# Kernel optimization log

Hardware: AMD Instinct MI355X
Metric: run time of the kernel (lower is better)

The kernel has to match this reference:

```python
import jax, jax.numpy as jnp
from jax import lax
import numpy as np

KS = 5
STRIDE = 4
SCALE = 10.0
PAD = 1        # conv_transpose2d padding (hardcoded in source)
OUT_PAD = 1    # output_padding
DN = ('NCHW', 'OIHW', 'NCHW')


def _same_pad(x, ks, stride):
    # torch same_padding: pad so out = ceil(H/stride)
    H, W = x.shape[-2], x.shape[-1]
    oh = -(-H // stride); ow = -(-W // stride)
    ph = max(0, (oh - 1) * stride + ks - H)
    pw = max(0, (ow - 1) * stride + ks - W)
    return jnp.pad(x, ((0, 0), (0, 0), (ph // 2, ph - ph // 2), (pw // 2, pw - pw // 2)))


def _patches(x, ks, stride):
    # torch extract_image_patches (same padding + unfold), returned as [N, L, C, ks, ks]
    N, C, H, W = x.shape
    oh = -(-H // stride); ow = -(-W // stride)
    xp = _same_pad(x, ks, stride)
    ys = (jnp.arange(oh) * stride)[:, None] + jnp.arange(ks)[None, :]   # [oh, ks]
    xs = (jnp.arange(ow) * stride)[:, None] + jnp.arange(ks)[None, :]   # [ow, ks]
    p = xp[:, :, ys, :][:, :, :, :, xs]   # [N, C, oh, ks, ow, ks]
    return p.transpose(0, 2, 4, 1, 3, 5).reshape(N, oh * ow, C, ks, ks)


def _conv3(x, W, b):
    # BasicBlock: 3x3 conv pad 1 + bias + LeakyReLU(0.01)
    y = lax.conv_general_dilated(x, W, (1, 1), [(1, 1), (1, 1)], dimension_numbers=DN)
    return jax.nn.leaky_relu(y + b[None, :, None, None], 0.01)


def _attend(qp, kp, vp):
    # qp: [C, Hp, Wp] padded query feature; kp: [L, C, ks, ks]; vp: [L, B, ks, ks]
    kmax = jnp.max(jnp.sqrt(jnp.sum(kp * kp, axis=(1, 2, 3))))
    kn = kp / kmax
    w = lax.conv_general_dilated(qp[None], kn, (STRIDE, STRIDE), 'VALID', dimension_numbers=DN)  # [1, L, h, w]
    wn = jax.nn.softmax(w * SCALE, axis=1)
    # conv_transpose2d(wn, vp, stride=4, padding=1, output_padding=1) as lhs-dilated conv
    ker = jnp.flip(vp.transpose(1, 0, 2, 3), (2, 3))  # [B, L, ks, ks]
    lo = KS - 1 - PAD
    hi = KS - 1 - PAD + OUT_PAD
    out = lax.conv_general_dilated(wn, ker, (1, 1), [(lo, hi), (lo, hi)],
                                   lhs_dilation=(STRIDE, STRIDE), dimension_numbers=DN)
    return out[0] / 6.0


def setup_inputs() -> dict:
    key = jax.random.key(0)
    k = jax.random.split(key, 12)
    N, CIN, MID, B = 8, 64, 64, 64
    H, HL = 256, 64
    s = 0.05
    return {
        'ms':   jax.random.normal(k[0], (N, B, HL, HL), jnp.float32),
        'pan':  jax.random.normal(k[1], (N, CIN, H, H), jnp.float32),
        'pan2': jax.random.normal(k[2], (N, CIN, HL, HL), jnp.float32),
        'Wq': jax.random.normal(k[3], (MID, CIN, 3, 3), jnp.float32) * s,
        'bq': jnp.zeros((MID,), jnp.float32),
        'Wk': jax.random.normal(k[4], (MID, CIN, 3, 3), jnp.float32) * s,
        'bk': jnp.zeros((MID,), jnp.float32),
        'Wv': jax.random.normal(k[5], (B, B, 3, 3), jnp.float32) * s,
        'bv': jnp.zeros((B,), jnp.float32),
        'Wr': jax.random.normal(k[6], (B, B, 3, 3), jnp.float32) * s,
        'br': jnp.zeros((B,), jnp.float32),
    }


def reference(ms, pan, pan2, Wq, bq, Wk, bk, Wv, bv, Wr, br):
    k_fea = _conv3(pan2, Wk, bk)               # [N, MID, 64, 64]
    k_patch = _patches(k_fea, KS, STRIDE)      # [N, L=256, MID, 5, 5]
    q_fea = _conv3(pan, Wq, bq)                # [N, MID, 256, 256]
    q_pad = _same_pad(q_fea, KS, STRIDE)       # [N, MID, 257, 257]
    v_fea = _conv3(ms, Wv, bv)                 # [N, B, 64, 64]
    v_patch = _patches(v_fea, KS, STRIDE)      # [N, L, B, 5, 5]
    res = jax.vmap(_attend)(q_pad, k_patch, v_patch)  # [N, B, 256, 256]
    return _conv3(res, Wr, br)
```

## Files before the change

### kernel.cpp

```cpp
#include <hip/hip_runtime.h>
#include <math.h>

#define NB   8
#define CI   64
#define COC  64
#define HQ   256
#define HK   64
#define KS   5
#define LL   256
#define NPAD 1664
#define QP2  (257 * 264)

typedef __attribute__((ext_vector_type(8))) short bf16x8s;
typedef __attribute__((ext_vector_type(4))) float f32x4;

static __device__ __forceinline__ unsigned short f2bf(float f) {
  union { float f; unsigned u; } v; v.f = f;
  unsigned r = v.u + 0x7FFF + ((v.u >> 16) & 1);
  return (unsigned short)(r >> 16);
}
static __device__ __forceinline__ float bf2f(unsigned short h) {
  union { unsigned u; float f; } v; v.u = ((unsigned)h) << 16; return v.f;
}

__global__ void wtrans8_kernel(const float* __restrict__ Wt, float* __restrict__ Wo) {
  const int co = threadIdx.x;
  const int tap = blockIdx.x;
  const int ci = blockIdx.y;
  Wo[(((co >> 3) * 64 + ci) * 9 + tap) * 8 + (co & 7)] = Wt[(co * 64 + ci) * 9 + tap];
}

__global__ void wtrans_mfma(const float* __restrict__ Wt, unsigned short* __restrict__ wimg) {
  const int ch = blockIdx.x;
  const int tap = ch >> 1, cih = ch & 1;
  for (int idx = threadIdx.x; idx < 64 * 40; idx += 256) {
    const int co = idx / 40, s = idx - co * 40;
    unsigned short v = 0;
    if (s < 32) v = f2bf(Wt[((size_t)co * 64 + cih * 32 + s) * 9 + tap]);
    wimg[(size_t)ch * 64 * 40 + idx] = v;
  }
}

__global__ void pad_copy(const float* __restrict__ src, float* __restrict__ dst,
                         int H, int W, int S, int total) {
  const int idx = blockIdx.x * 256 + threadIdx.x;
  if (idx >= total) return;
  const int p = idx / (H * W);
  const int rem = idx - p * H * W;
  const int y = rem / W, x = rem - y * W;
  dst[((size_t)p * (H + 2) + y + 1) * S + x + 1] = src[idx];
}

__global__ void border_zero(float* __restrict__ dst, int H, int W, int S) {
  const int p = blockIdx.x;
  float* b = dst + (size_t)p * (H + 2) * S;
  for (int c = threadIdx.x; c < S; c += 256) {
    b[c] = 0.f;
    b[(size_t)(H + 1) * S + c] = 0.f;
  }
  for (int r = 1 + threadIdx.x; r <= H; r += 256) {
    b[(size_t)r * S] = 0.f;
    b[(size_t)r * S + W + 1] = 0.f;
  }
}

__global__ void pad_rci(const float* __restrict__ src, unsigned short* __restrict__ dst) {
  const int ct = blockIdx.x, g = blockIdx.y, n = blockIdx.z;
  const int c0 = ct * 66;
  __shared__ float t[64 * 68];
  const int jl = threadIdx.x & 63, cg = threadIdx.x >> 6;
  const int row = g - 1;
  const bool rok = (row >= 0 && row < 256);
  for (int ci = cg; ci < 64; ci += 4) {
    #pragma unroll
    for (int jb = 0; jb < 2; ++jb) {
      const int j = jl + jb * 64;
      if (j < 66) {
        const int x = c0 - 1 + j;
        float v = 0.f;
        if (rok && x >= 0 && x < 256)
          v = src[(((size_t)n * 64 + ci) * 256 + row) * 256 + x];
        t[ci * 68 + j] = v;
      }
    }
  }
  __syncthreads();
  const int cil = threadIdx.x & 63, cc = threadIdx.x >> 6;
  unsigned short* db = dst + (((size_t)n * 258 + g) * 264) * 64;
  for (int c = cc; c < 66; c += 4)
    db[(size_t)(c0 + c) * 64 + cil] = f2bf(t[cil * 68 + c]);
}

__global__ void rbz(unsigned short* __restrict__ resbf) {
  const int n = blockIdx.x;
  unsigned short* b = resbf + (size_t)n * 258 * 264 * 64;
  for (int idx = threadIdx.x; idx < 264 * 64; idx += 256) {
    b[idx] = 0;
    b[(size_t)257 * 264 * 64 + idx] = 0;
  }
  for (int idx = threadIdx.x; idx < 256 * 64; idx += 256) {
    const int r = idx >> 6, ci = idx & 63;
    b[((size_t)(r + 1) * 264) * 64 + ci] = 0;
    b[((size_t)(r + 1) * 264 + 257) * 64 + ci] = 0;
  }
}

__global__ void qz(unsigned short* __restrict__ qhi, unsigned short* __restrict__ qlo) {
  const int n = blockIdx.x;
  unsigned short* bh = qhi + (size_t)n * QP2 * 64;
  unsigned short* bl = qlo + (size_t)n * QP2 * 64;
  for (int g = threadIdx.x; g < 4224; g += 256) {
    ((unsigned long long*)(bh + (size_t)256 * 264 * 64))[g] = 0ull;
    ((unsigned long long*)(bl + (size_t)256 * 264 * 64))[g] = 0ull;
  }
  for (int g = threadIdx.x; g < 4096; g += 256) {
    const int r = g >> 4, q = g & 15;
    const size_t off = ((size_t)r * 264 + 256) * 64 + q * 4;
    *(unsigned long long*)(bh + off) = 0ull;
    *(unsigned long long*)(bl + off) = 0ull;
  }
}

__global__ __launch_bounds__(256) void conv3m(
    const unsigned short* __restrict__ inbf,
    const unsigned short* __restrict__ wimg,
    const float* __restrict__ bias,
    float* __restrict__ out, int PS, int RS) {
  const int x0 = blockIdx.x * 64;
  const int y  = blockIdx.y;
  const int n  = blockIdx.z;
  const int tid = threadIdx.x;
  const int lane = tid & 63;
  const int wv = tid >> 6;
  const int col = lane & 15;
  const int kg  = lane >> 4;

  __shared__ unsigned short in_s[3 * 66 * 72];

  {
    const unsigned short* src = inbf + ((size_t)n * 258 + y) * 264 * 64;
    if (tid < 198) {
      const int r = tid / 66, c = tid - r * 66;
      const unsigned short* s = src + ((size_t)r * 264 + x0 + c) * 64;
      unsigned short* d = &in_s[(r * 66 + c) * 72];
      #pragma unroll
      for (int q = 0; q < 8; ++q)
        *(float4*)(d + q * 8) = *(const float4*)(s + q * 8);
    }
  }
  __syncthreads();

  f32x4 acc[4];
  #pragma unroll
  for (int p = 0; p < 4; ++p) acc[p] = (f32x4){0.f, 0.f, 0.f, 0.f};

  const unsigned short* wbase = wimg + ((size_t)(wv * 16 + col)) * 40 + kg * 8;

  #pragma unroll 2
  for (int ch = 0; ch < 18; ++ch) {
    const int tap = ch >> 1, cih = ch & 1;
    const int dy = tap / 3, dx = tap - dy * 3;
    const bf16x8s a = *(const bf16x8s*)(wbase + (size_t)ch * 64 * 40);
    const int cix = cih * 32 + kg * 8;
    #pragma unroll
    for (int p = 0; p < 4; ++p) {
      const int c = p * 16 + col + dx;
      const bf16x8s b = *(const bf16x8s*)&in_s[(dy * 66 + c) * 72 + cix];
      acc[p] = __builtin_amdgcn_mfma_f32_16x16x32_bf16(a, b, acc[p], 0, 0, 0);
    }
  }

  const int cobase = wv * 16 + kg * 4;
  const float4 bb = *(const float4*)&bias[cobase];
  const float bv[4] = {bb.x, bb.y, bb.z, bb.w};
  #pragma unroll
  for (int p = 0; p < 4; ++p) {
    const int x = x0 + p * 16 + col;
    #pragma unroll
    for (int r = 0; r < 4; ++r) {
      float t = acc[p][r] + bv[r];
      t = t > 0.f ? t : 0.01f * t;
      out[(size_t)(n * 64 + cobase + r) * PS + (size_t)y * RS + x] = t;
    }
  }
}

__global__ __launch_bounds__(256) void conv3mq(
    const unsigned short* __restrict__ inbf,
    const unsigned short* __restrict__ wimg,
    const float* __restrict__ bias,
    unsigned short* __restrict__ qhi, unsigned short* __restrict__ qlo) {
  const int x0 = blockIdx.x * 64;
  const int y  = blockIdx.y;
  const int n  = blockIdx.z;
  const int tid = threadIdx.x;
  const int lane = tid & 63;
  const int wv = tid >> 6;
  const int col = lane & 15;
  const int kg  = lane >> 4;

  __shared__ unsigned short in_s[3 * 66 * 72];

  {
    const unsigned short* src = inbf + ((size_t)n * 258 + y) * 264 * 64;
    if (tid < 198) {
      const int r = tid / 66, c = tid - r * 66;
      const unsigned short* s = src + ((size_t)r * 264 + x0 + c) * 64;
      unsigned short* d = &in_s[(r * 66 + c) * 72];
      #pragma unroll
      for (int q = 0; q < 8; ++q)
        *(float4*)(d + q * 8) = *(const float4*)(s + q * 8);
    }
  }
  __syncthreads();

  f32x4 acc[4];
  #pragma unroll
  for (int p = 0; p < 4; ++p) acc[p] = (f32x4){0.f, 0.f, 0.f, 0.f};

  const unsigned short* wbase = wimg + ((size_t)(wv * 16 + col)) * 40 + kg * 8;

  #pragma unroll 2
  for (int ch = 0; ch < 18; ++ch) {
    const int tap = ch >> 1, cih = ch & 1;
    const int dy = tap / 3, dx = tap - dy * 3;
    const bf16x8s a = *(const bf16x8s*)(wbase + (size_t)ch * 64 * 40);
    const int cix = cih * 32 + kg * 8;
    #pragma unroll
    for (int p = 0; p < 4; ++p) {
      const int c = p * 16 + col + dx;
      const bf16x8s b = *(const bf16x8s*)&in_s[(dy * 66 + c) * 72 + cix];
      acc[p] = __builtin_amdgcn_mfma_f32_16x16x32_bf16(a, b, acc[p], 0, 0, 0);
    }
  }

  const int cobase = wv * 16 + kg * 4;
  const float4 bb = *(const float4*)&bias[cobase];
  const float bv[4] = {bb.x, bb.y, bb.z, bb.w};
  unsigned short* hb = qhi + ((size_t)n * 257 + y) * 264 * 64;
  unsigned short* lb = qlo + ((size_t)n * 257 + y) * 264 * 64;
  #pragma unroll
  for (int p = 0; p < 4; ++p) {
    const int x = x0 + p * 16 + col;
    unsigned long long hp = 0, lp = 0;
    #pragma unroll
    for (int r = 0; r < 4; ++r) {
      float t = acc[p][r] + bv[r];
      t = t > 0.f ? t : 0.01f * t;
      const unsigned short h = f2bf(t);
      const unsigned short lo = f2bf(t - bf2f(h));
      hp |= ((unsigned long long)h) << (16 * r);
      lp |= ((unsigned long long)lo) << (16 * r);
    }
    *(unsigned long long*)(hb + (size_t)x * 64 + cobase) = hp;
    *(unsigned long long*)(lb + (size_t)x * 64 + cobase) = lp;
  }
}

__global__ __launch_bounds__(256) void conv3s(
    const float* __restrict__ inp, const float* __restrict__ Wts,
    const float* __restrict__ bias, float* __restrict__ out,
    int H, int Wd, int S, int outPS, int outRS) {
  const int x0 = blockIdx.x * 64;
  const int y0 = blockIdx.y * 8;
  const int z  = blockIdx.z;
  const int n  = z >> 3;
  const int cog = z & 7;
  const int tid = threadIdx.x;
  const int xq = tid & 15;
  const int yt = (tid >> 4) & 7;
  const int cg = tid >> 7;
  const int Hp = H + 2;

  __shared__ float in_s[10 * 72];
  __shared__ float w_s[CI * 9 * 8];

  {
    const float* wbase = Wts + (size_t)cog * (CI * 9 * 8);
    for (int idx = tid; idx < CI * 9 * 2; idx += 256)
      *(float4*)&w_s[idx * 4] = *(const float4*)(wbase + idx * 4);
  }

  float acc[4][4];
  #pragma unroll
  for (int a = 0; a < 4; ++a)
    #pragma unroll
    for (int b = 0; b < 4; ++b) acc[a][b] = 0.f;

  const bool hasA = tid < 180;
  const int arow = tid / 18, ac4 = tid - arow * 18;
  const float* gplane0 = inp + (size_t)(n * CI) * Hp * S;
  const size_t aoff = ((size_t)(y0 + arow)) * S + x0 + ac4 * 4;

  float4 sA = make_float4(0.f, 0.f, 0.f, 0.f);
  if (hasA) sA = *(const float4*)(gplane0 + aoff);

  for (int ci = 0; ci < CI; ++ci) {
    __syncthreads();
    if (hasA) *(float4*)&in_s[arow * 72 + ac4 * 4] = sA;
    if (ci + 1 < CI && hasA)
      sA = *(const float4*)(gplane0 + (size_t)(ci + 1) * Hp * S + aoff);
    __syncthreads();

    float xin[3][8];
    const int cb = xq * 4;
    #pragma unroll
    for (int r = 0; r < 3; ++r) {
      const float4 xa = *(const float4*)&in_s[(yt + r) * 72 + cb];
      const float4 xb = *(const float4*)&in_s[(yt + r) * 72 + cb + 4];
      xin[r][0] = xa.x; xin[r][1] = xa.y; xin[r][2] = xa.z; xin[r][3] = xa.w;
      xin[r][4] = xb.x; xin[r][5] = xb.y; xin[r][6] = xb.z; xin[r][7] = xb.w;
    }

    const float* wci = &w_s[(ci * 9) * 8 + cg * 4];
    #pragma unroll
    for (int ky = 0; ky < 3; ++ky) {
      #pragma unroll
      for (int kx = 0; kx < 3; ++kx) {
        const float4 w4 = *(const float4*)&wci[(ky * 3 + kx) * 8];
        const float wv[4] = {w4.x, w4.y, w4.z, w4.w};
        #pragma unroll
        for (int c = 0; c < 4; ++c)
          #pragma unroll
          for (int dx = 0; dx < 4; ++dx)
            acc[c][dx] = fmaf(wv[c], xin[ky][dx + kx], acc[c][dx]);
      }
    }
  }

  #pragma unroll
  for (int c = 0; c < 4; ++c) {
    const int co = cog * 8 + cg * 4 + c;
    const float bv = bias[co];
    float4 o;
    float t;
    t = acc[c][0] + bv; o.x = t > 0.f ? t : 0.01f * t;
    t = acc[c][1] + bv; o.y = t > 0.f ? t : 0.01f * t;
    t = acc[c][2] + bv; o.z = t > 0.f ? t : 0.01f * t;
    t = acc[c][3] + bv; o.w = t > 0.f ? t : 0.01f * t;
    *(float4*)(out + (size_t)(n * COC + co) * outPS + (size_t)(y0 + yt) * outRS + x0 + xq * 4) = o;
  }
}

__global__ void knorm_kernel(const float* __restrict__ kfea, float* __restrict__ norms) {
  const int l = blockIdx.x, n = blockIdx.y, c = threadIdx.x;
  const int ly = l >> 4, lx = l & 15;
  const float* base = kfea + ((size_t)(n * CI + c) * HK) * HK;
  float ss = 0.f;
  #pragma unroll
  for (int i = 0; i < KS; ++i) {
    const int r = 4 * ly + i;
    if (r >= HK) continue;
    #pragma unroll
    for (int j = 0; j < KS; ++j) {
      const int cc = 4 * lx + j;
      if (cc >= HK) continue;
      const float v = base[r * HK + cc];
      ss = fmaf(v, v, ss);
    }
  }
  for (int off = 32; off; off >>= 1) ss += __shfl_down(ss, off);
  if (c == 0) norms[n * LL + l] = ss;
}

__global__ void kscale_kernel(const float* __restrict__ norms, float* __restrict__ kscale) {
  const int n = blockIdx.x, t = threadIdx.x;
  float v = norms[n * LL + t];
  for (int off = 32; off; off >>= 1) v = fmaxf(v, __shfl_down(v, off));
  __shared__ float red[4];
  if ((t & 63) == 0) red[t >> 6] = v;
  __syncthreads();
  if (t == 0) {
    const float m = fmaxf(fmaxf(red[0], red[1]), fmaxf(red[2], red[3]));
    kscale[n] = 10.0f / sqrtf(m);
  }
}

__global__ void kp_gather2(const float* __restrict__ kfea, const float* __restrict__ kscale,
                           unsigned short* __restrict__ khi, unsigned short* __restrict__ klo) {
  const int tap = blockIdx.x, cih = blockIdx.y, n = blockIdx.z;
  const int s = threadIdx.x & 31, lg = threadIdx.x >> 5;
  const int i = tap / 5, j = tap % 5;
  const float sc = kscale[n];
  const float* kb = kfea + ((size_t)(n * 64 + cih * 32 + s) * 64) * 64;
  const size_t ob = (((size_t)n * 50 + tap * 2 + cih) * 256) * 32;
  for (int lb = 0; lb < 32; ++lb) {
    const int l = lb * 8 + lg;
    const int r = 4 * (l >> 4) + i, c = 4 * (l & 15) + j;
    float v = 0.f;
    if (r < 64 && c < 64) v = kb[r * 64 + c] * sc;
    const unsigned short h = f2bf(v);
    khi[ob + (size_t)l * 32 + s] = h;
    klo[ob + (size_t)l * 32 + s] = f2bf(v - bf2f(h));
  }
}

__global__ __launch_bounds__(512) void qk_fused(
    const unsigned short* __restrict__ qhi, const unsigned short* __restrict__ qlo,
    const unsigned short* __restrict__ khi, const unsigned short* __restrict__ klo,
    unsigned short* __restrict__ wnbf) {
  const int yb = blockIdx.x, n = blockIdx.y;
  const int tid = threadIdx.x;
  const int lane = tid & 63, wv = tid >> 6;
  const int qg = wv >> 2, lq = wv & 3;
  const int col = lane & 15, kg = lane >> 4;

  __shared__ float red[64][5];
  __shared__ float redm[64];

  f32x4 acc[2][4];
  #pragma unroll
  for (int fm = 0; fm < 2; ++fm)
    #pragma unroll
    for (int fn = 0; fn < 4; ++fn) acc[fm][fn] = (f32x4){0.f, 0.f, 0.f, 0.f};

  const unsigned short* khb = khi + (size_t)n * 50 * 8192;
  const unsigned short* klb = klo + (size_t)n * 50 * 8192;
  const unsigned short* qhb = qhi + (size_t)n * QP2 * 64;
  const unsigned short* qlb = qlo + (size_t)n * QP2 * 64;

  for (int ch = 0; ch < 50; ++ch) {
    const int tap = ch >> 1, cih = ch & 1;
    const int i = tap / 5, j = tap - 5 * i;
    bf16x8s ah[2], al[2];
    #pragma unroll
    for (int fm = 0; fm < 2; ++fm) {
      const size_t qoff = (((size_t)(4 * yb + i) * 264)
                          + 4 * (qg * 32 + fm * 16 + col) + j) * 64
                        + cih * 32 + kg * 8;
      ah[fm] = *(const bf16x8s*)(qhb + qoff);
      al[fm] = *(const bf16x8s*)(qlb + qoff);
    }
    #pragma unroll
    for (int fn = 0; fn < 4; ++fn) {
      const size_t boff = ((size_t)ch * 256 + lq * 64 + fn * 16 + col) * 32 + kg * 8;
      const bf16x8s bh = *(const bf16x8s*)(khb + boff);
      const bf16x8s bl = *(const bf16x8s*)(klb + boff);
      #pragma unroll
      for (int fm = 0; fm < 2; ++fm) {
        acc[fm][fn] = __builtin_amdgcn_mfma_f32_16x16x32_bf16(ah[fm], bh, acc[fm][fn], 0, 0, 0);
        acc[fm][fn] = __builtin_amdgcn_mfma_f32_16x16x32_bf16(ah[fm], bl, acc[fm][fn], 0, 0, 0);
        acc[fm][fn] = __builtin_amdgcn_mfma_f32_16x16x32_bf16(al[fm], bh, acc[fm][fn], 0, 0, 0);
      }
    }
  }

  #pragma unroll
  for (int fm = 0; fm < 2; ++fm)
    #pragma unroll
    for (int r = 0; r < 4; ++r) {
      float m = fmaxf(fmaxf(acc[fm][0][r], acc[fm][1][r]),
                      fmaxf(acc[fm][2][r], acc[fm][3][r]));
      #pragma unroll
      for (int off = 1; off < 16; off <<= 1) m = fmaxf(m, __shfl_xor(m, off));
      if (col == 0) red[qg * 32 + fm * 16 + kg * 4 + r][lq] = m;
    }
  __syncthreads();
  if (tid < 64) {
    const float bm = fmaxf(fmaxf(red[tid][0], red[tid][1]),
                           fmaxf(red[tid][2], red[tid][3]));
    redm[tid] = bm;
  }
  __syncthreads();
  #pragma unroll
  for (int fm = 0; fm < 2; ++fm)
    #pragma unroll
    for (int r = 0; r < 4; ++r) {
      const float bm = redm[qg * 32 + fm * 16 + kg * 4 + r];
      float s = 0.f;
      #pragma unroll
      for (int fn = 0; fn < 4; ++fn) {
        const float e = __expf(acc[fm][fn][r] - bm);
        acc[fm][fn][r] = e;
        s += e;
      }
      #pragma unroll
      for (int off = 1; off < 16; off <<= 1) s += __shfl_xor(s, off);
      if (col == 0) red[qg * 32 + fm * 16 + kg * 4 + r][lq] = s;
    }
  __syncthreads();
  if (tid < 64) {
    redm[tid] = 1.0f / (red[tid][0] + red[tid][1] + red[tid][2] + red[tid][3]);
  }
  __syncthreads();
  unsigned short* wb = wnbf + ((size_t)n * 4096 + (size_t)yb * 64) * 256;
  #pragma unroll
  for (int fm = 0; fm < 2; ++fm)
    #pragma unroll
    for (int r = 0; r < 4; ++r) {
      const int q = qg * 32 + fm * 16 + kg * 4 + r;
      const float inv = redm[q];
      #pragma unroll
      for (int fn = 0; fn < 4; ++fn)
        wb[(size_t)q * 256 + lq * 64 + fn * 16 + col] = f2bf(acc[fm][fn][r] * inv);
    }
}

__global__ void vpt_gather(const float* __restrict__ vfea, unsigned short* __restrict__ vpt) {
  const int l4 = threadIdx.x & 63, bj = threadIdx.x >> 6;
  const int bij = blockIdx.x * 4 + bj;
  const int n = blockIdx.y;
  const int ij = bij >> 6, b = bij & 63;
  unsigned short o[4] = {0, 0, 0, 0};
  if (ij < 25) {
    const int i = ij / 5, j = ij % 5;
    const int ly = l4 >> 2;
    const int r = 4 * ly + i;
    if (r < HK) {
      const float* base = vfea + ((size_t)(n * COC + b) * HK + r) * HK;
      #pragma unroll
      for (int e = 0; e < 4; ++e) {
        const int lx = (l4 & 3) * 4 + e;
        const int c = 4 * lx + j;
        if (c < HK) o[e] = f2bf(base[c]);
      }
    }
  }
  unsigned long long pack = (unsigned long long)o[0] | ((unsigned long long)o[1] << 16)
                          | ((unsigned long long)o[2] << 32) | ((unsigned long long)o[3] << 48);
  *(unsigned long long*)(vpt + ((size_t)n * NPAD + bij) * 256 + l4 * 4) = pack;
}

__global__ __launch_bounds__(256) void pv_mfma(
    const unsigned short* __restrict__ wnb, const unsigned short* __restrict__ vpt,
    unsigned short* __restrict__ C0) {
  const int nz = blockIdx.z;
  const unsigned short* A = wnb + (size_t)nz * 4096 * 256;
  const unsigned short* B = vpt + (size_t)nz * NPAD * 256;
  unsigned short* C = C0 + (size_t)nz * 4096 * NPAD;
  const int m0 = blockIdx.x * 64;
  const int n0 = blockIdx.y * 128;
  const int tid = threadIdx.x;
  const int lane = tid & 63;
  const int wv = tid >> 6;
  const int wm = wv >> 1, wn_ = wv & 1;
  const int col = lane & 15, kg = lane >> 4;

  __shared__ unsigned short A_s[64 * 40];
  __shared__ unsigned short B_s[128 * 40];

  f32x4 acc[2][4];
  #pragma unroll
  for (int fm = 0; fm < 2; ++fm)
    #pragma unroll
    for (int fn = 0; fn < 4; ++fn) acc[fm][fn] = (f32x4){0.f, 0.f, 0.f, 0.f};

  for (int k0 = 0; k0 < 256; k0 += 32) {
    __syncthreads();
    {
      const int row = tid >> 2, q = tid & 3;
      *(float4*)&A_s[row * 40 + q * 8] =
          *(const float4*)&A[(size_t)(m0 + row) * 256 + k0 + q * 8];
    }
    {
      const int row = tid >> 1, hh = tid & 1;
      *(float4*)&B_s[row * 40 + hh * 16] =
          *(const float4*)&B[(size_t)(n0 + row) * 256 + k0 + hh * 16];
      *(float4*)&B_s[row * 40 + hh * 16 + 8] =
          *(const float4*)&B[(size_t)(n0 + row) * 256 + k0 + hh * 16 + 8];
    }
    __syncthreads();

    bf16x8s a[2], b[4];
    #pragma unroll
    for (int fm = 0; fm < 2; ++fm)
      a[fm] = *(const bf16x8s*)&A_s[(wm * 32 + fm * 16 + col) * 40 + kg * 8];
    #pragma unroll
    for (int fn = 0; fn < 4; ++fn)
      b[fn] = *(const bf16x8s*)&B_s[(wn_ * 64 + fn * 16 + col) * 40 + kg * 8];
    #pragma unroll
    for (int fm = 0; fm < 2; ++fm)
      #pragma unroll
      for (int fn = 0; fn < 4; ++fn)
        acc[fm][fn] = __builtin_amdgcn_mfma_f32_16x16x32_bf16(a[fm], b[fn], acc[fm][fn], 0, 0, 0);
  }

  #pragma unroll
  for (int fm = 0; fm < 2; ++fm) {
    #pragma unroll
    for (int fn = 0; fn < 4; ++fn) {
      const int cg = n0 + wn_ * 64 + fn * 16 + col;
      #pragma unroll
      for (int r = 0; r < 4; ++r) {
        const int rg = m0 + wm * 32 + fm * 16 + kg * 4 + r;
        C[(size_t)rg * NPAD + cg] = f2bf(acc[fm][fn][r]);
      }
    }
  }
}

__global__ __launch_bounds__(256) void u_scatter(
    const unsigned short* __restrict__ U0, unsigned short* __restrict__ resbf, int n0) {
  const int n = n0 + blockIdx.z;
  const unsigned short* U = U0 + (size_t)blockIdx.z * 4096 * NPAD;
  const int y = blockIdx.y;
  const int xt = blockIdx.x;
  const int tid = threadIdx.x;
  __shared__ float t_lds[64][65];
  const int ym = (y + 1) >> 2, yr = (y + 1) & 3;
  const bool v0 = (ym < 64);
  const bool v1 = (yr == 0 && ym >= 1);
  const int b = tid & 63, xg = tid >> 6;
  for (int xi = 0; xi < 16; ++xi) {
    const int x = xt * 64 + xg * 16 + xi;
    const int xm = (x + 1) >> 2, xr = (x + 1) & 3;
    const bool u0 = (xm < 64);
    const bool u1 = (xr == 0 && xm >= 1);
    float s = 0.f;
    if (v0) {
      const size_t rb = (size_t)(ym * 64) * NPAD;
      if (u0) s += bf2f(U[rb + (size_t)xm * NPAD + (yr * 5 + xr) * 64 + b]);
      if (u1) s += bf2f(U[rb + (size_t)(xm - 1) * NPAD + (yr * 5 + 4) * 64 + b]);
    }
    if (v1) {
      const size_t rb = (size_t)((ym - 1) * 64) * NPAD;
      if (u0) s += bf2f(U[rb + (size_t)xm * NPAD + (4 * 5 + xr) * 64 + b]);
      if (u1) s += bf2f(U[rb + (size_t)(xm - 1) * NPAD + (4 * 5 + 4) * 64 + b]);
    }
    t_lds[xg * 16 + xi][b] = s * (1.0f / 6.0f);
  }
  __syncthreads();
  unsigned short* db = resbf + (((size_t)n * 258 + (y + 1)) * 264) * 64;
  for (int xi = 0; xi < 16; ++xi) {
    const int x = xg * 16 + xi;
    db[(size_t)(xt * 64 + x + 1) * 64 + b] = f2bf(t_lds[x][b]);
  }
}

extern "C" void kernel_launch(void* const* d_in, const int* in_sizes, int n_in,
                              void* d_out, int out_size, void* d_ws, size_t ws_size,
                              hipStream_t stream) {
  const float* ms   = (const float*)d_in[0];
  const float* pan  = (const float*)d_in[1];
  const float* pan2 = (const float*)d_in[2];
  const float* Wq   = (const float*)d_in[3];
  const float* bq   = (const float*)d_in[4];
  const float* Wk   = (const float*)d_in[5];
  const float* bk   = (const float*)d_in[6];
  const float* Wv   = (const float*)d_in[7];
  const float* bv   = (const float*)d_in[8];
  const float* Wr   = (const float*)d_in[9];
  const float* br   = (const float*)d_in[10];
  float* out = (float*)d_out;

  float* ws = (float*)d_ws;
  const size_t SZ_QP  = (size_t)NB * CI * QP2;
  const size_t SZ_K   = (size_t)NB * CI * HK * HK;
  const size_t SZ_WN  = (size_t)NB * 64 * 64 * LL;
  const size_t SZ_VPT = (size_t)NB * NPAD * 256 / 2;
  const size_t SZ_KP  = (size_t)NB * 50 * 256 * 32;
  const size_t SZ_PS  = (size_t)NB * CI * 66 * 72;
  const size_t SZ_WI  = 23040;
  const size_t SZ_U1F = (size_t)4096 * NPAD / 2;
  const size_t SZ_UAF = (size_t)NB * SZ_U1F;

  float* q_pad   = ws;
  float* k_fea   = q_pad + SZ_QP;
  float* v_fea   = k_fea + SZ_K;
  float* wnbf_f  = v_fea + SZ_K;
  float* vptbf_f = wnbf_f + SZ_WN / 2;
  float* kp      = vptbf_f + SZ_VPT;
  float* norms   = kp + SZ_KP;
  float* kscale  = norms + NB * LL;
  float* wtk     = kscale + 64;
  float* wtv     = wtk + 36864;
  float* wimgqf  = wtv + 36864;
  float* wimgrf  = wimgqf + SZ_WI;
  float* ms_pad  = wimgrf + SZ_WI;
  float* pan2pad = ms_pad + SZ_PS;
  float* tail    = pan2pad + SZ_PS;

  unsigned short* qhi  = (unsigned short*)q_pad;
  unsigned short* qlo  = qhi + (size_t)NB * QP2 * 64;
  unsigned short* khi  = (unsigned short*)kp;
  unsigned short* klo  = khi + (size_t)NB * 50 * 256 * 32;
  unsigned short* wimgq = (unsigned short*)wimgqf;
  unsigned short* wimgr = (unsigned short*)wimgrf;
  unsigned short* wnbf  = (unsigned short*)wnbf_f;
  unsigned short* vptbf = (unsigned short*)vptbf_f;
  unsigned short* panbf = (unsigned short*)tail;
  unsigned short* U     = (unsigned short*)tail;
  unsigned short* resbf = (unsigned short*)q_pad;

  const size_t base_elems = (size_t)(tail - ws);
  const bool batched = ws_size >= (base_elems + SZ_UAF) * sizeof(float);

  wtrans8_kernel<<<dim3(9, 64), 64, 0, stream>>>(Wk, wtk);
  wtrans8_kernel<<<dim3(9, 64), 64, 0, stream>>>(Wv, wtv);
  wtrans_mfma<<<dim3(18), 256, 0, stream>>>(Wq, wimgq);
  wtrans_mfma<<<dim3(18), 256, 0, stream>>>(Wr, wimgr);

  {
    const int totS = NB * CI * HK * HK;
    pad_copy<<<dim3((totS + 255) / 256), 256, 0, stream>>>(ms, ms_pad, HK, HK, 72, totS);
    pad_copy<<<dim3((totS + 255) / 256), 256, 0, stream>>>(pan2, pan2pad, HK, HK, 72, totS);
    border_zero<<<dim3(NB * CI), 256, 0, stream>>>(ms_pad, HK, HK, 72);
    border_zero<<<dim3(NB * CI), 256, 0, stream>>>(pan2pad, HK, HK, 72);
    pad_rci<<<dim3(4, 258, NB), 256, 0, stream>>>(pan, panbf);
  }

  conv3s<<<dim3(HK / 64, HK / 8, NB * 8), 256, 0, stream>>>(pan2pad, wtk, bk, k_fea, HK, HK, 72, HK * HK, HK);
  conv3s<<<dim3(HK / 64, HK / 8, NB * 8), 256, 0, stream>>>(ms_pad,  wtv, bv, v_fea, HK, HK, 72, HK * HK, HK);
  conv3mq<<<dim3(4, 256, NB), 256, 0, stream>>>(panbf, wimgq, bq, qhi, qlo);
  qz<<<dim3(NB), 256, 0, stream>>>(qhi, qlo);

  knorm_kernel<<<dim3(LL, NB), 64, 0, stream>>>(k_fea, norms);
  kscale_kernel<<<NB, 256, 0, stream>>>(norms, kscale);

  kp_gather2<<<dim3(25, 2, NB), 256, 0, stream>>>(k_fea, kscale, khi, klo);

  qk_fused<<<dim3(64, NB), 512, 0, stream>>>(qhi, qlo, khi, klo, wnbf);

  rbz<<<dim3(NB), 256, 0, stream>>>(resbf);

  vpt_gather<<<dim3(NPAD / 4, NB), 256, 0, stream>>>(v_fea, vptbf);

  if (batched) {
    pv_mfma<<<dim3(64, 13, NB), 256, 0, stream>>>(wnbf, vptbf, U);
    u_scatter<<<dim3(4, HQ, NB), 256, 0, stream>>>(U, resbf, 0);
  } else {
    for (int n = 0; n < NB; ++n) {
      pv_mfma<<<dim3(64, 13, 1), 256, 0, stream>>>(wnbf + (size_t)n * 4096 * 256,
                                                   vptbf + (size_t)n * NPAD * 256, U);
      u_scatter<<<dim3(4, HQ, 1), 256, 0, stream>>>(U, resbf, n);
    }
  }

  conv3m<<<dim3(4, 256, NB), 256, 0, stream>>>(resbf, wimgr, br, out, HQ * HQ, HQ);
}
```

Baseline: 769.3 us.

## Split QK reduction across wave groups with LDS partial-sum combine

Changes the qk_fused work split. Each group of four waves now covers all 64 query positions but only half of the 50 reduction chunks, instead of half the queries over all chunks. Each wave then reuses every K fragment across four query tiles instead of two, which halves the K global loads per MFMA. The two partial accumulators are summed through a 66KB LDS buffer. The cost is more accumulator registers, heavy LDS use that may lower occupancy, and a softmax phase that runs on only half the waves.

```diff
diff --git a/kernel.cpp b/kernel.cpp
--- a/kernel.cpp
+++ b/kernel.cpp
@@ -402,15 +402,16 @@
   const int yb = blockIdx.x, n = blockIdx.y;
   const int tid = threadIdx.x;
   const int lane = tid & 63, wv = tid >> 6;
-  const int qg = wv >> 2, lq = wv & 3;
+  const int kh = wv >> 2, lq = wv & 3;
   const int col = lane & 15, kg = lane >> 4;
 
+  __shared__ float sc_s[64 * 260];
   __shared__ float red[64][5];
   __shared__ float redm[64];
 
-  f32x4 acc[2][4];
-  #pragma unroll
-  for (int fm = 0; fm < 2; ++fm)
+  f32x4 acc[4][4];
+  #pragma unroll
+  for (int fm = 0; fm < 4; ++fm)
     #pragma unroll
     for (int fn = 0; fn < 4; ++fn) acc[fm][fn] = (f32x4){0.f, 0.f, 0.f, 0.f};
 
@@ -419,14 +420,15 @@
   const unsigned short* qhb = qhi + (size_t)n * QP2 * 64;
   const unsigned short* qlb = qlo + (size_t)n * QP2 * 64;
 
-  for (int ch = 0; ch < 50; ++ch) {
+  const int ch0 = kh * 25;
+  for (int cc = 0; cc < 25; ++cc) {
+    const int ch = ch0 + cc;
     const int tap = ch >> 1, cih = ch & 1;
     const int i = tap / 5, j = tap - 5 * i;
-    bf16x8s ah[2], al[2];
-    #pragma unroll
-    for (int fm = 0; fm < 2; ++fm) {
-      const size_t qoff = (((size_t)(4 * yb + i) * 264)
-                          + 4 * (qg * 32 + fm * 16 + col) + j) * 64
+    bf16x8s ah[4], al[4];
+    #pragma unroll
+    for (int fm = 0; fm < 4; ++fm) {
+      const size_t qoff = (((size_t)(4 * yb + i) * 264) + 4 * (fm * 16 + col) + j) * 64
                         + cih * 32 + kg * 8;
       ah[fm] = *(const bf16x8s*)(qhb + qoff);
       al[fm] = *(const bf16x8s*)(qlb + qoff);
@@ -437,7 +439,7 @@
       const bf16x8s bh = *(const bf16x8s*)(khb + boff);
       const bf16x8s bl = *(const bf16x8s*)(klb + boff);
       #pragma unroll
-      for (int fm = 0; fm < 2; ++fm) {
+      for (int fm = 0; fm < 4; ++fm) {
         acc[fm][fn] = __builtin_amdgcn_mfma_f32_16x16x32_bf16(ah[fm], bh, acc[fm][fn], 0, 0, 0);
         acc[fm][fn] = __builtin_amdgcn_mfma_f32_16x16x32_bf16(ah[fm], bl, acc[fm][fn], 0, 0, 0);
         acc[fm][fn] = __builtin_amdgcn_mfma_f32_16x16x32_bf16(al[fm], bh, acc[fm][fn], 0, 0, 0);
@@ -445,55 +447,78 @@
     }
   }
 
-  #pragma unroll
-  for (int fm = 0; fm < 2; ++fm)
-    #pragma unroll
-    for (int r = 0; r < 4; ++r) {
-      float m = fmaxf(fmaxf(acc[fm][0][r], acc[fm][1][r]),
-                      fmaxf(acc[fm][2][r], acc[fm][3][r]));
-      #pragma unroll
-      for (int off = 1; off < 16; off <<= 1) m = fmaxf(m, __shfl_xor(m, off));
-      if (col == 0) red[qg * 32 + fm * 16 + kg * 4 + r][lq] = m;
-    }
+  if (kh == 1) {
+    #pragma unroll
+    for (int fm = 0; fm < 4; ++fm)
+      #pragma unroll
+      for (int fn = 0; fn < 4; ++fn)
+        #pragma unroll
+        for (int r = 0; r < 4; ++r)
+          sc_s[(fm * 16 + kg * 4 + r) * 260 + lq * 64 + fn * 16 + col] = acc[fm][fn][r];
+  }
+  __syncthreads();
+  if (kh == 0) {
+    #pragma unroll
+    for (int fm = 0; fm < 4; ++fm)
+      #pragma unroll
+      for (int fn = 0; fn < 4; ++fn)
+        #pragma unroll
+        for (int r = 0; r < 4; ++r)
+          acc[fm][fn][r] += sc_s[(fm * 16 + kg * 4 + r) * 260 + lq * 64 + fn * 16 + col];
+
+    #pragma unroll
+    for (int fm = 0; fm < 4; ++fm)
+      #pragma unroll
+      for (int r = 0; r < 4; ++r) {
+        float m = fmaxf(fmaxf(acc[fm][0][r], acc[fm][1][r]),
+                        fmaxf(acc[fm][2][r], acc[fm][3][r]));
+        #pragma unroll
+        for (int off = 1; off < 16; off <<= 1) m = fmaxf(m, __shfl_xor(m, off));
+        if (col == 0) red[fm * 16 + kg * 4 + r][lq] = m;
+      }
+  }
   __syncthreads();
   if (tid < 64) {
-    const float bm = fmaxf(fmaxf(red[tid][0], red[tid][1]),
-                           fmaxf(red[tid][2], red[tid][3]));
-    redm[tid] = bm;
-  }
-  __syncthreads();
-  #pragma unroll
-  for (int fm = 0; fm < 2; ++fm)
-    #pragma unroll
-    for (int r = 0; r < 4; ++r) {
-      const float bm = redm[qg * 32 + fm * 16 + kg * 4 + r];
-      float s = 0.f;
-      #pragma unroll
-      for (int fn = 0; fn < 4; ++fn) {
-        const float e = __expf(acc[fm][fn][r] - bm);
-        acc[fm][fn][r] = e;
-        s += e;
+    redm[tid] = fmaxf(fmaxf(red[tid][0], red[tid][1]),
+                      fmaxf(red[tid][2], red[tid][3]));
+  }
+  __syncthreads();
+  if (kh == 0) {
+    #pragma unroll
+    for (int fm = 0; fm < 4; ++fm)
+      #pragma unroll
+      for (int r = 0; r < 4; ++r) {
+        const float bm = redm[fm * 16 + kg * 4 + r];
+        float s = 0.f;
+        #pragma unroll
+        for (int fn = 0; fn < 4; ++fn) {
+          const float e = __expf(acc[fm][fn][r] - bm);
+          acc[fm][fn][r] = e;
+          s += e;
+        }
+        #pragma unroll
+        for (int off = 1; off < 16; off <<= 1) s += __shfl_xor(s, off);
+        if (col == 0) red[fm * 16 + kg * 4 + r][lq] = s;
       }
-      #pragma unroll
-      for (int off = 1; off < 16; off <<= 1) s += __shfl_xor(s, off);
-      if (col == 0) red[qg * 32 + fm * 16 + kg * 4 + r][lq] = s;
-    }
+  }
   __syncthreads();
   if (tid < 64) {
     redm[tid] = 1.0f / (red[tid][0] + red[tid][1] + red[tid][2] + red[tid][3]);
   }
   __syncthreads();
-  unsigned short* wb = wnbf + ((size_t)n * 4096 + (size_t)yb * 64) * 256;
-  #pragma unroll
-  for (int fm = 0; fm < 2; ++fm)
-    #pragma unroll
-    for (int r = 0; r < 4; ++r) {
-      const int q = qg * 32 + fm * 16 + kg * 4 + r;
-      const float inv = redm[q];
-      #pragma unroll
-      for (int fn = 0; fn < 4; ++fn)
-        wb[(size_t)q * 256 + lq * 64 + fn * 16 + col] = f2bf(acc[fm][fn][r] * inv);
-    }
+  if (kh == 0) {
+    unsigned short* wb = wnbf + ((size_t)n * 4096 + (size_t)yb * 64) * 256;
+    #pragma unroll
+    for (int fm = 0; fm < 4; ++fm)
+      #pragma unroll
+      for (int r = 0; r < 4; ++r) {
+        const int q = fm * 16 + kg * 4 + r;
+        const float inv = redm[q];
+        #pragma unroll
+        for (int fn = 0; fn < 4; ++fn)
+          wb[(size_t)q * 256 + lq * 64 + fn * 16 + col] = f2bf(acc[fm][fn][r] * inv);
+      }
+  }
 }
 
 __global__ void vpt_gather(const float* __restrict__ vfea, unsigned short* __restrict__ vpt) {
```

Result: faster. 747.7 us (-2.8%).
